# Kernel optimization log

Hardware: AMD Instinct MI355X
Metric: run time of the kernel (lower is better)

The kernel has to match this reference:

```python
import jax, jax.numpy as jnp
import numpy as np

DIM = 384
NUM_HEADS = 6
HEAD_DIM = DIM // NUM_HEADS
SCALE = HEAD_DIM ** -0.5


def setup_inputs() -> dict:
    key = jax.random.key(0)
    k_x, k_qkvw, k_qkvb, k_pw, k_pb = jax.random.split(key, 5)
    B, N, C = 8, 2048, DIM
    x = jax.random.normal(k_x, (B, N, C), dtype=jnp.float32)
    # nn.Linear weights stored as (out, in); apply as x @ W.T + b
    s = 1.0 / np.sqrt(C)
    qkv_w = jax.random.uniform(k_qkvw, (3 * C, C), minval=-s, maxval=s, dtype=jnp.float32)
    qkv_b = jax.random.uniform(k_qkvb, (3 * C,), minval=-s, maxval=s, dtype=jnp.float32)
    proj_w = jax.random.uniform(k_pw, (C, C), minval=-s, maxval=s, dtype=jnp.float32)
    proj_b = jax.random.uniform(k_pb, (C,), minval=-s, maxval=s, dtype=jnp.float32)
    return {"x": x, "qkv_w": qkv_w, "qkv_b": qkv_b, "proj_w": proj_w,
            "proj_b": proj_b, "h": 64, "w": 32}


def reference(x, qkv_w, qkv_b, proj_w, proj_b, h, w):
    B, N, C = x.shape
    H, D = NUM_HEADS, HEAD_DIM
    qkv = x @ qkv_w.T + qkv_b              # [B, N, 3C]
    qkv = qkv.reshape(B, N, 3, H, D)
    q = qkv[:, :, 0].transpose(0, 2, 1, 3) * SCALE  # [B, H, N, D]
    k = qkv[:, :, 1].transpose(0, 2, 1, 3)
    v = qkv[:, :, 2].transpose(0, 2, 1, 3)
    attn = jnp.einsum('bhnd,bhmd->bhnm', q, k)      # [B, H, N, N]
    attn = jax.nn.softmax(attn, axis=-1)
    out = jnp.einsum('bhnm,bhmd->bhnd', attn, v)    # [B, H, N, D]
    out = out.transpose(0, 2, 1, 3).reshape(B, N, C)
    return out @ proj_w.T + proj_b
```

## Files before the change

### kernel.cpp

```cpp
#include <hip/hip_runtime.h>

typedef __attribute__((ext_vector_type(8))) short bf16x8;
typedef __attribute__((ext_vector_type(4))) float f32x4;
typedef __attribute__((ext_vector_type(16))) float f32x16;
typedef __attribute__((ext_vector_type(4))) unsigned int u32x4;

#define DIMC 384
#define NHEADS 6
#define HDIM 64
#define BATCH 8
#define SEQ 2048
#define TOKENS (BATCH*SEQ)
#define QKV_OUT (3*DIMC)

__device__ __forceinline__ unsigned short f2bf(float f) {
  unsigned int u = __float_as_uint(f);
  u += 0x7fffu + ((u >> 16) & 1u);
  return (unsigned short)(u >> 16);
}

__device__ __forceinline__ unsigned int cvt_pk_bf16(float a, float b) {
  unsigned int r;
  asm volatile("v_cvt_pk_bf16_f32 %0, %1, %2" : "=v"(r) : "v"(a), "v"(b));
  return r;
}

__device__ __forceinline__ void async_load16(const void* g, void* l) {
  __builtin_amdgcn_global_load_lds(
      (const __attribute__((address_space(1))) unsigned int*)g,
      (__attribute__((address_space(3))) unsigned int*)l, 16, 0, 0);
}

#define N4_X   (TOKENS*DIMC/4)
#define N4_W1  (QKV_OUT*DIMC/4)
#define N4_W2  (DIMC*DIMC/4)
__global__ void cast3_kernel(const float* __restrict__ x,
                             const float* __restrict__ w1,
                             const float* __restrict__ w2,
                             unsigned short* __restrict__ ox,
                             unsigned short* __restrict__ o1,
                             unsigned short* __restrict__ o2) {
  int i = blockIdx.x * blockDim.x + threadIdx.x;
  const int stride = gridDim.x * blockDim.x;
  for (; i < N4_X + N4_W1 + N4_W2; i += stride) {
    const float* src; unsigned short* dst; int j = i;
    if (j < N4_X)            { src = x;  dst = ox; }
    else if (j < N4_X+N4_W1) { j -= N4_X; src = w1; dst = o1; }
    else                     { j -= N4_X+N4_W1; src = w2; dst = o2; }
    float4 v = ((const float4*)src)[j];
    ushort4 o;
    o.x = f2bf(v.x); o.y = f2bf(v.y); o.z = f2bf(v.z); o.w = f2bf(v.w);
    ((ushort4*)dst)[j] = o;
  }
}

__global__ __launch_bounds__(256) void qkv_gemm_kernel(
    const unsigned short* __restrict__ A,
    const unsigned short* __restrict__ W,
    const float* __restrict__ bias,
    unsigned short* __restrict__ Qb,
    unsigned short* __restrict__ Kb,
    unsigned short* __restrict__ Vtb) {
  __shared__ unsigned short As[3][128*32];
  __shared__ unsigned short Bs[3][128*32];
  const int tid = threadIdx.x;
  const int w = tid >> 6, l = tid & 63;
  const int wm = w >> 1, wn = w & 1;
  const int q4 = l >> 4, r15 = l & 15;
  const int wg = blockIdx.x;
  const int logical = (wg & 7) * 144 + (wg >> 3);
  const int row = logical / 9, col = logical % 9;
  const int m0 = row * 128;
  const int n0 = col * 128;

  f32x4 acc[4][4];
#pragma unroll
  for (int i = 0; i < 4; i++)
#pragma unroll
    for (int j = 0; j < 4; j++) acc[i][j] = f32x4{0.f, 0.f, 0.f, 0.f};

  const int arow = l >> 2;
  const int achk = l & 3;
  const unsigned short* Asrc = A + (size_t)(m0 + w*16 + arow) * 384 + achk * 8;
  const unsigned short* Wsrc = W + (size_t)(n0 + w*16 + arow) * 384 + achk * 8;

#pragma unroll
  for (int cc = 0; cc < 2; ++cc) {
    async_load16(Asrc + cc*64*384, (char*)&As[0][0] + cc*4096 + w*1024);
    async_load16(Wsrc + cc*64*384, (char*)&Bs[0][0] + cc*4096 + w*1024);
  }

  int cur = 0;
  for (int kt = 0; kt < 12; ++kt) {
    const int nxt = (cur == 2) ? 0 : cur + 1;
    if (kt < 11) {
#pragma unroll
      for (int cc = 0; cc < 2; ++cc) {
        async_load16(Asrc + (kt+1)*32 + cc*64*384, (char*)&As[0][0] + nxt*8192 + cc*4096 + w*1024);
        async_load16(Wsrc + (kt+1)*32 + cc*64*384, (char*)&Bs[0][0] + nxt*8192 + cc*4096 + w*1024);
      }
      asm volatile("s_waitcnt vmcnt(4)" ::: "memory");
    } else {
      asm volatile("s_waitcnt vmcnt(0)" ::: "memory");
    }
    __builtin_amdgcn_s_barrier();
    asm volatile("" ::: "memory");
    const unsigned short* asb = &As[0][0] + cur*4096;
    const unsigned short* bsb = &Bs[0][0] + cur*4096;
    bf16x8 a[4], b[4];
#pragma unroll
    for (int mi = 0; mi < 4; mi++)
      a[mi] = *(const bf16x8*)(asb + (wm*64 + mi*16 + r15)*32 + q4*8);
#pragma unroll
    for (int ni = 0; ni < 4; ni++)
      b[ni] = *(const bf16x8*)(bsb + (wn*64 + ni*16 + r15)*32 + q4*8);
    __builtin_amdgcn_s_setprio(1);
#pragma unroll
    for (int mi = 0; mi < 4; mi++)
#pragma unroll
      for (int ni = 0; ni < 4; ni++)
        acc[mi][ni] = __builtin_amdgcn_mfma_f32_16x16x32_bf16(
            a[mi], b[ni], acc[mi][ni], 0, 0, 0);
    __builtin_amdgcn_s_setprio(0);
    cur = nxt;
  }
  const int c3 = col / 3;
  const int nrel0 = (col % 3) * 128 + wn * 64;
  if (c3 == 2) {
#pragma unroll
    for (int ni = 0; ni < 4; ni++) {
      int ncol = nrel0 + ni*16 + r15;
      float bv = bias[n0 + wn*64 + ni*16 + r15];
      int h = ncol >> 6, d = ncol & 63;
#pragma unroll
      for (int mi = 0; mi < 4; mi++) {
        int m = m0 + wm*64 + mi*16 + 4*q4;
        int bb = m >> 11, t = m & 2047;
        ushort4 pk;
        pk.x = f2bf(acc[mi][ni][0] + bv);
        pk.y = f2bf(acc[mi][ni][1] + bv);
        pk.z = f2bf(acc[mi][ni][2] + bv);
        pk.w = f2bf(acc[mi][ni][3] + bv);
        *(ushort4*)(Vtb + ((size_t)(bb*NHEADS + h)*HDIM + d)*SEQ + t) = pk;
      }
    }
  } else {
    unsigned short* D = (c3 == 0) ? Qb : Kb;
    const float scale = (c3 == 0) ? 0.125f * 1.4426950408889634f : 1.0f;
#pragma unroll
    for (int ni = 0; ni < 4; ni++) {
      int ncol = nrel0 + ni*16 + r15;
      float bv = bias[n0 + wn*64 + ni*16 + r15];
      int h = ncol >> 6, d = ncol & 63;
#pragma unroll
      for (int mi = 0; mi < 4; mi++) {
#pragma unroll
        for (int reg = 0; reg < 4; reg++) {
          int m = m0 + wm*64 + mi*16 + 4*q4 + reg;
          int bb = m >> 11, t = m & 2047;
          float v = (acc[mi][ni][reg] + bv) * scale;
          D[((size_t)(bb*NHEADS + h)*SEQ + t)*HDIM + d] = f2bf(v);
        }
      }
    }
  }
}

__global__ __launch_bounds__(256, 3) void flash_kernel(
    const unsigned short* __restrict__ Q, const unsigned short* __restrict__ K,
    const unsigned short* __restrict__ Vt, unsigned short* __restrict__ O2) {
  __shared__ unsigned short Ks[3][64*64];
  __shared__ unsigned short Vs[3][64*64];
  const int tid = threadIdx.x;
  const int w = tid >> 6, l = tid & 63;
  const int hl = l >> 5, l31 = l & 31, l7 = l & 7;
  const int wg = blockIdx.x;
  const int logical = (wg & 7) * 96 + (wg >> 3);
  const int qt = logical & 15, bh = logical >> 4;
  const unsigned short* Qp = Q  + (size_t)bh * SEQ * HDIM;
  const unsigned short* Kp = K  + (size_t)bh * SEQ * HDIM;
  const unsigned short* Vp = Vt + (size_t)bh * HDIM * SEQ;

  const int qrow = qt*128 + w*32 + l31;
  bf16x8 qf[4];
#pragma unroll
  for (int ks = 0; ks < 4; ks++)
    qf[ks] = *(const bf16x8*)(Qp + (size_t)qrow*HDIM + ks*16 + hl*8);

  const int srow = w*8 + (l >> 3);
  const int sch  = l7 ^ (l >> 3) ^ w;
  const unsigned short* Ksrc = Kp + (size_t)srow*HDIM + sch*8;
  const unsigned short* Vsrc = Vp + (size_t)srow*SEQ  + sch*8;

  const int swl = (l31 >> 3) & 3;
  int rdoff[4];
#pragma unroll
  for (int ks = 0; ks < 4; ks++)
    rdoff[ks] = l31*128 + (((ks*2 + hl) ^ l7 ^ swl) << 4);

  f32x16 o0 = {}, o1 = {};
  float l_run = 0.f;

  async_load16(Ksrc,           (char*)&Ks[0][0] + w*1024);
  async_load16(Ksrc + 32*HDIM, (char*)&Ks[0][0] + w*1024 + 4096);
  async_load16(Vsrc,           (char*)&Vs[0][0] + w*1024);
  async_load16(Vsrc + 32*SEQ,  (char*)&Vs[0][0] + w*1024 + 4096);

  int cur = 0;
  for (int kt = 0; kt < 32; ++kt) {
    const int nxt = (cur == 2) ? 0 : cur + 1;
    if (kt < 31) {
      const unsigned short* ks_ = Ksrc + (size_t)(kt+1)*64*HDIM;
      const unsigned short* vs_ = Vsrc + (size_t)(kt+1)*64;
      char* kd = (char*)&Ks[0][0] + nxt*8192 + w*1024;
      char* vd = (char*)&Vs[0][0] + nxt*8192 + w*1024;
      async_load16(ks_,           kd);
      async_load16(ks_ + 32*HDIM, kd + 4096);
      async_load16(vs_,           vd);
      async_load16(vs_ + 32*SEQ,  vd + 4096);
      asm volatile("s_waitcnt vmcnt(4)" ::: "memory");
    } else {
      asm volatile("s_waitcnt vmcnt(0)" ::: "memory");
    }
    __builtin_amdgcn_s_barrier();
    asm volatile("" ::: "memory");

    const char* ksb = (const char*)&Ks[0][0] + cur*8192;
    const char* vsb = (const char*)&Vs[0][0] + cur*8192;

    bf16x8 pa0, pa1;
    float lsumA;
    {
      f32x16 s = {};
      __builtin_amdgcn_s_setprio(1);
#pragma unroll
      for (int ks = 0; ks < 4; ks++) {
        bf16x8 kf = *(const bf16x8*)(ksb + rdoff[ks]);
        s = __builtin_amdgcn_mfma_f32_32x32x16_bf16(kf, qf[ks], s, 0, 0, 0);
      }
      __builtin_amdgcn_s_setprio(0);
      unsigned int Y[4][2];
      float lsum = 0.f;
#pragma unroll
      for (int h = 0; h < 4; h++) {
        float a0 = __builtin_amdgcn_exp2f(s[4*h+0]);
        float a1 = __builtin_amdgcn_exp2f(s[4*h+1]);
        float a2 = __builtin_amdgcn_exp2f(s[4*h+2]);
        float a3 = __builtin_amdgcn_exp2f(s[4*h+3]);
        lsum += (a0+a1)+(a2+a3);
        Y[h][0] = cvt_pk_bf16(a0, a1);
        Y[h][1] = cvt_pk_bf16(a2, a3);
      }
      lsumA = lsum;
      {
        unsigned int x0 = Y[0][0], x1 = Y[0][1], y0 = Y[1][0], y1 = Y[1][1];
        asm volatile("v_permlane32_swap_b32 %0, %1" : "+v"(x0), "+v"(y0));
        asm volatile("v_permlane32_swap_b32 %0, %1" : "+v"(x1), "+v"(y1));
        u32x4 t; t[0] = x0; t[1] = x1; t[2] = y0; t[3] = y1;
        union { u32x4 u; bf16x8 b; } cvt; cvt.u = t;
        pa0 = cvt.b;
      }
      {
        unsigned int x0 = Y[2][0], x1 = Y[2][1], y0 = Y[3][0], y1 = Y[3][1];
        asm volatile("v_permlane32_swap_b32 %0, %1" : "+v"(x0), "+v"(y0));
        asm volatile("v_permlane32_swap_b32 %0, %1" : "+v"(x1), "+v"(y1));
        u32x4 t; t[0] = x0; t[1] = x1; t[2] = y0; t[3] = y1;
        union { u32x4 u; bf16x8 b; } cvt; cvt.u = t;
        pa1 = cvt.b;
      }
    }
    __builtin_amdgcn_sched_barrier(0);

    bf16x8 pa2, pa3;
    float lsumB;
    {
      f32x16 s = {};
      __builtin_amdgcn_s_setprio(1);
#pragma unroll
      for (int ks = 0; ks < 4; ks++) {
        bf16x8 kf = *(const bf16x8*)(ksb + 4096 + rdoff[ks]);
        s = __builtin_amdgcn_mfma_f32_32x32x16_bf16(kf, qf[ks], s, 0, 0, 0);
      }
      __builtin_amdgcn_s_setprio(0);
      unsigned int Y[4][2];
      float lsum = 0.f;
#pragma unroll
      for (int h = 0; h < 4; h++) {
        float a0 = __builtin_amdgcn_exp2f(s[4*h+0]);
        float a1 = __builtin_amdgcn_exp2f(s[4*h+1]);
        float a2 = __builtin_amdgcn_exp2f(s[4*h+2]);
        float a3 = __builtin_amdgcn_exp2f(s[4*h+3]);
        lsum += (a0+a1)+(a2+a3);
        Y[h][0] = cvt_pk_bf16(a0, a1);
        Y[h][1] = cvt_pk_bf16(a2, a3);
      }
      lsumB = lsum;
      {
        unsigned int x0 = Y[0][0], x1 = Y[0][1], y0 = Y[1][0], y1 = Y[1][1];
        asm volatile("v_permlane32_swap_b32 %0, %1" : "+v"(x0), "+v"(y0));
        asm volatile("v_permlane32_swap_b32 %0, %1" : "+v"(x1), "+v"(y1));
        u32x4 t; t[0] = x0; t[1] = x1; t[2] = y0; t[3] = y1;
        union { u32x4 u; bf16x8 b; } cvt; cvt.u = t;
        pa2 = cvt.b;
      }
      {
        unsigned int x0 = Y[2][0], x1 = Y[2][1], y0 = Y[3][0], y1 = Y[3][1];
        asm volatile("v_permlane32_swap_b32 %0, %1" : "+v"(x0), "+v"(y0));
        asm volatile("v_permlane32_swap_b32 %0, %1" : "+v"(x1), "+v"(y1));
        u32x4 t; t[0] = x0; t[1] = x1; t[2] = y0; t[3] = y1;
        union { u32x4 u; bf16x8 b; } cvt; cvt.u = t;
        pa3 = cvt.b;
      }
    }
    l_run += lsumA + lsumB;
    __builtin_amdgcn_sched_barrier(0);

    __builtin_amdgcn_s_setprio(1);
    {
      bf16x8 vf0 = *(const bf16x8*)(vsb + rdoff[0]);
      bf16x8 vf1 = *(const bf16x8*)(vsb + 4096 + rdoff[0]);
      o0 = __builtin_amdgcn_mfma_f32_32x32x16_bf16(pa0, vf0, o0, 0, 0, 0);
      o1 = __builtin_amdgcn_mfma_f32_32x32x16_bf16(pa0, vf1, o1, 0, 0, 0);
      vf0 = *(const bf16x8*)(vsb + rdoff[1]);
      vf1 = *(const bf16x8*)(vsb + 4096 + rdoff[1]);
      o0 = __builtin_amdgcn_mfma_f32_32x32x16_bf16(pa1, vf0, o0, 0, 0, 0);
      o1 = __builtin_amdgcn_mfma_f32_32x32x16_bf16(pa1, vf1, o1, 0, 0, 0);
      vf0 = *(const bf16x8*)(vsb + rdoff[2]);
      vf1 = *(const bf16x8*)(vsb + 4096 + rdoff[2]);
      o0 = __builtin_amdgcn_mfma_f32_32x32x16_bf16(pa2, vf0, o0, 0, 0, 0);
      o1 = __builtin_amdgcn_mfma_f32_32x32x16_bf16(pa2, vf1, o1, 0, 0, 0);
      vf0 = *(const bf16x8*)(vsb + rdoff[3]);
      vf1 = *(const bf16x8*)(vsb + 4096 + rdoff[3]);
      o0 = __builtin_amdgcn_mfma_f32_32x32x16_bf16(pa3, vf0, o0, 0, 0, 0);
      o1 = __builtin_amdgcn_mfma_f32_32x32x16_bf16(pa3, vf1, o1, 0, 0, 0);
    }
    __builtin_amdgcn_s_setprio(0);
    cur = nxt;
  }

  l_run += __shfl_xor(l_run, 32, 64);
  const float linv = 1.0f / l_run;
  const int b = bh / NHEADS, h = bh % NHEADS;
#pragma unroll
  for (int reg = 0; reg < 16; reg++) {
    const int qr = (reg & 3) + 8*(reg >> 2) + 4*hl;
    const float lr = __shfl(linv, qr, 64);
    const int t = qt*128 + w*32 + qr;
    unsigned short* dst = O2 + ((size_t)(b*SEQ + t))*DIMC + h*HDIM;
    dst[l31]      = f2bf(o0[reg] * lr);
    dst[32 + l31] = f2bf(o1[reg] * lr);
  }
}

__global__ __launch_bounds__(256) void proj_gemm_kernel(
    const unsigned short* __restrict__ A,
    const unsigned short* __restrict__ W,
    const float* __restrict__ bias,
    float* __restrict__ out) {
  __shared__ unsigned short As[2][128*32];
  __shared__ unsigned short Bs[2][64*32];
  const int tid = threadIdx.x;
  const int w = tid >> 6, l = tid & 63;
  const int q4 = l >> 4, r15 = l & 15;
  const int wg = blockIdx.x;
  const int logical = (wg & 7) * 96 + (wg >> 3);
  const int row = logical / 6, col = logical % 6;
  const int m0 = row * 128;
  const int n0 = col * 64;

  f32x4 acc[2][4];
#pragma unroll
  for (int i = 0; i < 2; i++)
#pragma unroll
    for (int j = 0; j < 4; j++) acc[i][j] = f32x4{0.f, 0.f, 0.f, 0.f};

  const int arow = l >> 2;
  const int achk = l & 3;
  const unsigned short* Asrc = A + (size_t)(m0 + w*16 + arow) * 384 + achk * 8;
  const unsigned short* Wsrc = W + (size_t)(n0 + w*16 + arow) * 384 + achk * 8;

#pragma unroll
  for (int cc = 0; cc < 2; ++cc)
    async_load16(Asrc + cc*64*384, (char*)As[0] + cc*4096 + w*1024);
  async_load16(Wsrc, (char*)Bs[0] + w*1024);

  for (int kt = 0; kt < 12; ++kt) {
    const int buf = kt & 1;
    if (kt < 11) {
#pragma unroll
      for (int cc = 0; cc < 2; ++cc)
        async_load16(Asrc + (kt+1)*32 + cc*64*384, (char*)As[buf^1] + cc*4096 + w*1024);
      async_load16(Wsrc + (kt+1)*32, (char*)Bs[buf^1] + w*1024);
      asm volatile("s_waitcnt vmcnt(3)" ::: "memory");
    } else {
      asm volatile("s_waitcnt vmcnt(0)" ::: "memory");
    }
    __builtin_amdgcn_s_barrier();
    asm volatile("" ::: "memory");
    bf16x8 a[2], b[4];
#pragma unroll
    for (int mi = 0; mi < 2; mi++)
      a[mi] = *(const bf16x8*)(&As[buf][(w*32 + mi*16 + r15)*32 + q4*8]);
#pragma unroll
    for (int ni = 0; ni < 4; ni++)
      b[ni] = *(const bf16x8*)(&Bs[buf][(ni*16 + r15)*32 + q4*8]);
    __builtin_amdgcn_s_setprio(1);
#pragma unroll
    for (int mi = 0; mi < 2; mi++)
#pragma unroll
      for (int ni = 0; ni < 4; ni++)
        acc[mi][ni] = __builtin_amdgcn_mfma_f32_16x16x32_bf16(
            a[mi], b[ni], acc[mi][ni], 0, 0, 0);
    __builtin_amdgcn_s_setprio(0);
    asm volatile("s_waitcnt lgkmcnt(0)" ::: "memory");
    __builtin_amdgcn_s_barrier();
    asm volatile("" ::: "memory");
  }
#pragma unroll
  for (int ni = 0; ni < 4; ni++) {
    int ncol = n0 + ni*16 + r15;
    float bv = bias[ncol];
#pragma unroll
    for (int mi = 0; mi < 2; mi++) {
#pragma unroll
      for (int reg = 0; reg < 4; reg++) {
        int m = m0 + w*32 + mi*16 + 4*q4 + reg;
        out[(size_t)m * DIMC + ncol] = acc[mi][ni][reg] + bv;
      }
    }
  }
}

extern "C" void kernel_launch(void* const* d_in, const int* in_sizes, int n_in,
                              void* d_out, int out_size, void* d_ws, size_t ws_size,
                              hipStream_t stream) {
  const float* x      = (const float*)d_in[0];
  const float* qkv_w  = (const float*)d_in[1];
  const float* qkv_b  = (const float*)d_in[2];
  const float* proj_w = (const float*)d_in[3];
  const float* proj_b = (const float*)d_in[4];
  float* out = (float*)d_out;

  unsigned short* xbf   = (unsigned short*)d_ws;
  unsigned short* wqkv  = xbf   + (size_t)TOKENS * DIMC;
  unsigned short* wproj = wqkv  + (size_t)QKV_OUT * DIMC;
  unsigned short* Qb    = wproj + (size_t)DIMC * DIMC;
  unsigned short* Kb    = Qb    + (size_t)TOKENS * DIMC;
  unsigned short* Vtb   = Kb    + (size_t)TOKENS * DIMC;
  unsigned short* A2    = Vtb   + (size_t)TOKENS * DIMC;

  cast3_kernel<<<2048, 256, 0, stream>>>(x, qkv_w, proj_w, xbf, wqkv, wproj);
  qkv_gemm_kernel<<<1152, 256, 0, stream>>>(xbf, wqkv, qkv_b, Qb, Kb, Vtb);
  flash_kernel<<<768, 256, 0, stream>>>(Qb, Kb, Vtb, A2);
  proj_gemm_kernel<<<768, 256, 0, stream>>>(A2, wproj, proj_b, out);
}
```

Baseline: 114.4 us.

## Fuse x bf16 cast into QKV GEMM and load V fragments directly from global

The separate cast pass over x is removed. The QKV GEMM now async-loads fp32 x tiles into a swizzled LDS buffer and converts them to bf16 as it reads fragments, which saves a full write and read of the activation copy but doubles A-tile LDS size. The flash kernel drops its V shared-memory staging and loads V^T fragments straight from global into registers each iteration. V^T rows are padded to 2080 elements to avoid partition conflicts. The trade-off is more global-load latency inside the loop and higher register pressure in the flash kernel.

```diff
diff --git a/kernel.cpp b/kernel.cpp
--- a/kernel.cpp
+++ b/kernel.cpp
@@ -12,6 +12,7 @@
 #define SEQ 2048
 #define TOKENS (BATCH*SEQ)
 #define QKV_OUT (3*DIMC)
+#define VTP 2080
 
 __device__ __forceinline__ unsigned short f2bf(float f) {
   unsigned int u = __float_as_uint(f);
@@ -31,22 +32,18 @@
       (__attribute__((address_space(3))) unsigned int*)l, 16, 0, 0);
 }
 
-#define N4_X   (TOKENS*DIMC/4)
 #define N4_W1  (QKV_OUT*DIMC/4)
 #define N4_W2  (DIMC*DIMC/4)
-__global__ void cast3_kernel(const float* __restrict__ x,
-                             const float* __restrict__ w1,
+__global__ void castw_kernel(const float* __restrict__ w1,
                              const float* __restrict__ w2,
-                             unsigned short* __restrict__ ox,
                              unsigned short* __restrict__ o1,
                              unsigned short* __restrict__ o2) {
   int i = blockIdx.x * blockDim.x + threadIdx.x;
   const int stride = gridDim.x * blockDim.x;
-  for (; i < N4_X + N4_W1 + N4_W2; i += stride) {
+  for (; i < N4_W1 + N4_W2; i += stride) {
     const float* src; unsigned short* dst; int j = i;
-    if (j < N4_X)            { src = x;  dst = ox; }
-    else if (j < N4_X+N4_W1) { j -= N4_X; src = w1; dst = o1; }
-    else                     { j -= N4_X+N4_W1; src = w2; dst = o2; }
+    if (j < N4_W1) { src = w1; dst = o1; }
+    else           { j -= N4_W1; src = w2; dst = o2; }
     float4 v = ((const float4*)src)[j];
     ushort4 o;
     o.x = f2bf(v.x); o.y = f2bf(v.y); o.z = f2bf(v.z); o.w = f2bf(v.w);
@@ -55,13 +52,13 @@
 }
 
 __global__ __launch_bounds__(256) void qkv_gemm_kernel(
-    const unsigned short* __restrict__ A,
+    const float* __restrict__ A,
     const unsigned short* __restrict__ W,
     const float* __restrict__ bias,
     unsigned short* __restrict__ Qb,
     unsigned short* __restrict__ Kb,
     unsigned short* __restrict__ Vtb) {
-  __shared__ unsigned short As[3][128*32];
+  __shared__ float          Asf[3][128*32];
   __shared__ unsigned short Bs[3][128*32];
   const int tid = threadIdx.x;
   const int w = tid >> 6, l = tid & 63;
@@ -79,38 +76,55 @@
 #pragma unroll
     for (int j = 0; j < 4; j++) acc[i][j] = f32x4{0.f, 0.f, 0.f, 0.f};
 
-  const int arow = l >> 2;
-  const int achk = l & 3;
-  const unsigned short* Asrc = A + (size_t)(m0 + w*16 + arow) * 384 + achk * 8;
-  const unsigned short* Wsrc = W + (size_t)(n0 + w*16 + arow) * 384 + achk * 8;
-
-#pragma unroll
-  for (int cc = 0; cc < 2; ++cc) {
-    async_load16(Asrc + cc*64*384, (char*)&As[0][0] + cc*4096 + w*1024);
+  const int arow8 = l >> 3;
+  const int ag    = (l & 7) ^ arow8;
+  const float* Asrc = A + (size_t)(m0 + w*32 + arow8) * 384 + ag*4;
+  const int brow = l >> 2, bchk = l & 3;
+  const unsigned short* Wsrc = W + (size_t)(n0 + w*16 + brow) * 384 + bchk*8;
+
+#pragma unroll
+  for (int j = 0; j < 4; ++j)
+    async_load16(Asrc + j*8*384, (char*)&Asf[0][0] + w*4096 + j*1024);
+#pragma unroll
+  for (int cc = 0; cc < 2; ++cc)
     async_load16(Wsrc + cc*64*384, (char*)&Bs[0][0] + cc*4096 + w*1024);
-  }
 
   int cur = 0;
   for (int kt = 0; kt < 12; ++kt) {
     const int nxt = (cur == 2) ? 0 : cur + 1;
     if (kt < 11) {
 #pragma unroll
-      for (int cc = 0; cc < 2; ++cc) {
-        async_load16(Asrc + (kt+1)*32 + cc*64*384, (char*)&As[0][0] + nxt*8192 + cc*4096 + w*1024);
-        async_load16(Wsrc + (kt+1)*32 + cc*64*384, (char*)&Bs[0][0] + nxt*8192 + cc*4096 + w*1024);
-      }
-      asm volatile("s_waitcnt vmcnt(4)" ::: "memory");
+      for (int j = 0; j < 4; ++j)
+        async_load16(Asrc + (kt+1)*32 + j*8*384,
+                     (char*)&Asf[0][0] + nxt*16384 + w*4096 + j*1024);
+#pragma unroll
+      for (int cc = 0; cc < 2; ++cc)
+        async_load16(Wsrc + (kt+1)*32 + cc*64*384,
+                     (char*)&Bs[0][0] + nxt*8192 + cc*4096 + w*1024);
+      asm volatile("s_waitcnt vmcnt(6)" ::: "memory");
     } else {
       asm volatile("s_waitcnt vmcnt(0)" ::: "memory");
     }
     __builtin_amdgcn_s_barrier();
     asm volatile("" ::: "memory");
-    const unsigned short* asb = &As[0][0] + cur*4096;
+    const char* asb = (const char*)&Asf[0][0] + cur*16384;
     const unsigned short* bsb = &Bs[0][0] + cur*4096;
     bf16x8 a[4], b[4];
 #pragma unroll
-    for (int mi = 0; mi < 4; mi++)
-      a[mi] = *(const bf16x8*)(asb + (wm*64 + mi*16 + r15)*32 + q4*8);
+    for (int mi = 0; mi < 4; mi++) {
+      const int arow = wm*64 + mi*16 + r15;
+      const int p0 = (2*q4)     ^ (r15 & 7);
+      const int p1 = (2*q4 + 1) ^ (r15 & 7);
+      f32x4 lo = *(const f32x4*)(asb + arow*128 + p0*16);
+      f32x4 hi = *(const f32x4*)(asb + arow*128 + p1*16);
+      u32x4 t;
+      t[0] = cvt_pk_bf16(lo[0], lo[1]);
+      t[1] = cvt_pk_bf16(lo[2], lo[3]);
+      t[2] = cvt_pk_bf16(hi[0], hi[1]);
+      t[3] = cvt_pk_bf16(hi[2], hi[3]);
+      union { u32x4 u; bf16x8 v; } cvt; cvt.u = t;
+      a[mi] = cvt.v;
+    }
 #pragma unroll
     for (int ni = 0; ni < 4; ni++)
       b[ni] = *(const bf16x8*)(bsb + (wn*64 + ni*16 + r15)*32 + q4*8);
@@ -141,7 +155,7 @@
         pk.y = f2bf(acc[mi][ni][1] + bv);
         pk.z = f2bf(acc[mi][ni][2] + bv);
         pk.w = f2bf(acc[mi][ni][3] + bv);
-        *(ushort4*)(Vtb + ((size_t)(bb*NHEADS + h)*HDIM + d)*SEQ + t) = pk;
+        *(ushort4*)(Vtb + ((size_t)(bb*NHEADS + h)*HDIM + d)*VTP + t) = pk;
       }
     }
   } else {
@@ -170,7 +184,6 @@
     const unsigned short* __restrict__ Q, const unsigned short* __restrict__ K,
     const unsigned short* __restrict__ Vt, unsigned short* __restrict__ O2) {
   __shared__ unsigned short Ks[3][64*64];
-  __shared__ unsigned short Vs[3][64*64];
   const int tid = threadIdx.x;
   const int w = tid >> 6, l = tid & 63;
   const int hl = l >> 5, l31 = l & 31, l7 = l & 7;
@@ -179,7 +192,7 @@
   const int qt = logical & 15, bh = logical >> 4;
   const unsigned short* Qp = Q  + (size_t)bh * SEQ * HDIM;
   const unsigned short* Kp = K  + (size_t)bh * SEQ * HDIM;
-  const unsigned short* Vp = Vt + (size_t)bh * HDIM * SEQ;
+  const unsigned short* Vp = Vt + (size_t)bh * HDIM * VTP;
 
   const int qrow = qt*128 + w*32 + l31;
   bf16x8 qf[4];
@@ -190,7 +203,9 @@
   const int srow = w*8 + (l >> 3);
   const int sch  = l7 ^ (l >> 3) ^ w;
   const unsigned short* Ksrc = Kp + (size_t)srow*HDIM + sch*8;
-  const unsigned short* Vsrc = Vp + (size_t)srow*SEQ  + sch*8;
+
+  const unsigned short* vrow0 = Vp + (size_t)l31*VTP      + hl*8;
+  const unsigned short* vrow1 = Vp + (size_t)(32+l31)*VTP + hl*8;
 
   const int swl = (l31 >> 3) & 3;
   int rdoff[4];
@@ -203,30 +218,29 @@
 
   async_load16(Ksrc,           (char*)&Ks[0][0] + w*1024);
   async_load16(Ksrc + 32*HDIM, (char*)&Ks[0][0] + w*1024 + 4096);
-  async_load16(Vsrc,           (char*)&Vs[0][0] + w*1024);
-  async_load16(Vsrc + 32*SEQ,  (char*)&Vs[0][0] + w*1024 + 4096);
 
   int cur = 0;
   for (int kt = 0; kt < 32; ++kt) {
     const int nxt = (cur == 2) ? 0 : cur + 1;
+    bf16x8 vf0[4], vf1[4];
+#pragma unroll
+    for (int ks = 0; ks < 4; ks++) {
+      vf0[ks] = *(const bf16x8*)(vrow0 + kt*64 + ks*16);
+      vf1[ks] = *(const bf16x8*)(vrow1 + kt*64 + ks*16);
+    }
     if (kt < 31) {
       const unsigned short* ks_ = Ksrc + (size_t)(kt+1)*64*HDIM;
-      const unsigned short* vs_ = Vsrc + (size_t)(kt+1)*64;
       char* kd = (char*)&Ks[0][0] + nxt*8192 + w*1024;
-      char* vd = (char*)&Vs[0][0] + nxt*8192 + w*1024;
       async_load16(ks_,           kd);
       async_load16(ks_ + 32*HDIM, kd + 4096);
-      async_load16(vs_,           vd);
-      async_load16(vs_ + 32*SEQ,  vd + 4096);
-      asm volatile("s_waitcnt vmcnt(4)" ::: "memory");
+      asm volatile("s_waitcnt vmcnt(10)" ::: "memory");
     } else {
-      asm volatile("s_waitcnt vmcnt(0)" ::: "memory");
+      asm volatile("s_waitcnt vmcnt(8)" ::: "memory");
     }
     __builtin_amdgcn_s_barrier();
     asm volatile("" ::: "memory");
 
     const char* ksb = (const char*)&Ks[0][0] + cur*8192;
-    const char* vsb = (const char*)&Vs[0][0] + cur*8192;
 
     bf16x8 pa0, pa1;
     float lsumA;
@@ -316,24 +330,14 @@
     __builtin_amdgcn_sched_barrier(0);
 
     __builtin_amdgcn_s_setprio(1);
-    {
-      bf16x8 vf0 = *(const bf16x8*)(vsb + rdoff[0]);
-      bf16x8 vf1 = *(const bf16x8*)(vsb + 4096 + rdoff[0]);
-      o0 = __builtin_amdgcn_mfma_f32_32x32x16_bf16(pa0, vf0, o0, 0, 0, 0);
-      o1 = __builtin_amdgcn_mfma_f32_32x32x16_bf16(pa0, vf1, o1, 0, 0, 0);
-      vf0 = *(const bf16x8*)(vsb + rdoff[1]);
-      vf1 = *(const bf16x8*)(vsb + 4096 + rdoff[1]);
-      o0 = __builtin_amdgcn_mfma_f32_32x32x16_bf16(pa1, vf0, o0, 0, 0, 0);
-      o1 = __builtin_amdgcn_mfma_f32_32x32x16_bf16(pa1, vf1, o1, 0, 0, 0);
-      vf0 = *(const bf16x8*)(vsb + rdoff[2]);
-      vf1 = *(const bf16x8*)(vsb + 4096 + rdoff[2]);
-      o0 = __builtin_amdgcn_mfma_f32_32x32x16_bf16(pa2, vf0, o0, 0, 0, 0);
-      o1 = __builtin_amdgcn_mfma_f32_32x32x16_bf16(pa2, vf1, o1, 0, 0, 0);
-      vf0 = *(const bf16x8*)(vsb + rdoff[3]);
-      vf1 = *(const bf16x8*)(vsb + 4096 + rdoff[3]);
-      o0 = __builtin_amdgcn_mfma_f32_32x32x16_bf16(pa3, vf0, o0, 0, 0, 0);
-      o1 = __builtin_amdgcn_mfma_f32_32x32x16_bf16(pa3, vf1, o1, 0, 0, 0);
-    }
+    o0 = __builtin_amdgcn_mfma_f32_32x32x16_bf16(pa0, vf0[0], o0, 0, 0, 0);
+    o1 = __builtin_amdgcn_mfma_f32_32x32x16_bf16(pa0, vf1[0], o1, 0, 0, 0);
+    o0 = __builtin_amdgcn_mfma_f32_32x32x16_bf16(pa1, vf0[1], o0, 0, 0, 0);
+    o1 = __builtin_amdgcn_mfma_f32_32x32x16_bf16(pa1, vf1[1], o1, 0, 0, 0);
+    o0 = __builtin_amdgcn_mfma_f32_32x32x16_bf16(pa2, vf0[2], o0, 0, 0, 0);
+    o1 = __builtin_amdgcn_mfma_f32_32x32x16_bf16(pa2, vf1[2], o1, 0, 0, 0);
+    o0 = __builtin_amdgcn_mfma_f32_32x32x16_bf16(pa3, vf0[3], o0, 0, 0, 0);
+    o1 = __builtin_amdgcn_mfma_f32_32x32x16_bf16(pa3, vf1[3], o1, 0, 0, 0);
     __builtin_amdgcn_s_setprio(0);
     cur = nxt;
   }
@@ -441,16 +445,15 @@
   const float* proj_b = (const float*)d_in[4];
   float* out = (float*)d_out;
 
-  unsigned short* xbf   = (unsigned short*)d_ws;
-  unsigned short* wqkv  = xbf   + (size_t)TOKENS * DIMC;
+  unsigned short* wqkv  = (unsigned short*)d_ws;
   unsigned short* wproj = wqkv  + (size_t)QKV_OUT * DIMC;
   unsigned short* Qb    = wproj + (size_t)DIMC * DIMC;
   unsigned short* Kb    = Qb    + (size_t)TOKENS * DIMC;
   unsigned short* Vtb   = Kb    + (size_t)TOKENS * DIMC;
-  unsigned short* A2    = Vtb   + (size_t)TOKENS * DIMC;
-
-  cast3_kernel<<<2048, 256, 0, stream>>>(x, qkv_w, proj_w, xbf, wqkv, wproj);
-  qkv_gemm_kernel<<<1152, 256, 0, stream>>>(xbf, wqkv, qkv_b, Qb, Kb, Vtb);
+  unsigned short* A2    = Vtb   + (size_t)48 * HDIM * VTP;
+
+  castw_kernel<<<576, 256, 0, stream>>>(qkv_w, proj_w, wqkv, wproj);
+  qkv_gemm_kernel<<<1152, 256, 0, stream>>>(x, wqkv, qkv_b, Qb, Kb, Vtb);
   flash_kernel<<<768, 256, 0, stream>>>(Qb, Kb, Vtb, A2);
   proj_gemm_kernel<<<768, 256, 0, stream>>>(A2, wproj, proj_b, out);
 }
```

Measured after the change: 145.3 us. 1.27x slower.
